# Kernel optimization log

Hardware: AMD Instinct MI355X
Metric: run time of the kernel (lower is better)

The kernel has to match this reference:

```python
import jax, jax.numpy as jnp
import numpy as np

N_NODES = 100000
N_EDGES = 1600000
D_IN = 128
D_HID = 128
N_LAYERS = 3


def setup_inputs() -> dict:
    key = jax.random.key(0)
    k1, k2, k3, k4 = jax.random.split(key, 4)
    x = jax.random.normal(k1, (N_NODES, D_IN), dtype=jnp.float32)
    edge_index = jax.random.randint(k2, (2, N_EDGES), 0, N_NODES, dtype=jnp.int64)
    # Glorot-ish scale for stability across 3 layers
    Ws = jax.random.normal(k3, (N_LAYERS, D_IN, D_HID), dtype=jnp.float32) * (1.0 / np.sqrt(D_IN))
    bs = jax.random.normal(k4, (N_LAYERS, D_HID), dtype=jnp.float32) * 0.01
    return {"x": x, "edge_index": edge_index, "Ws": Ws, "bs": bs}


def _gcn_conv(x, row, col, deg_inv_sqrt, W, b, n_nodes):
    # Linear transform first (PyG GCNConv), then gather-normalize-scatter.
    h = x @ W                                        # [N, D]
    norm = deg_inv_sqrt[row] * deg_inv_sqrt[col]     # [E+N] (self-loops included)
    msg = h[row] * norm[:, None]                     # gather + scale, [E+N, D]
    out = jax.ops.segment_sum(msg, col, num_segments=n_nodes)  # scatter-add
    return out + b


def reference(x, edge_index, Ws, bs):
    n = x.shape[0]
    # add self-loops once (same for every layer)
    loop = jnp.arange(n, dtype=edge_index.dtype)
    row = jnp.concatenate([edge_index[0], loop])
    col = jnp.concatenate([edge_index[1], loop])
    # symmetric normalization: deg over target nodes (incl. self-loops)
    deg = jax.ops.segment_sum(jnp.ones_like(col, dtype=x.dtype), col, num_segments=n)
    deg_inv_sqrt = jnp.where(deg > 0, jax.lax.rsqrt(jnp.maximum(deg, 1.0)), 0.0)
    h = x
    for i in range(Ws.shape[0]):
        h = jax.nn.relu(_gcn_conv(h, row, col, deg_inv_sqrt, Ws[i], bs[i], n))
    return h
```

## Files before the change

### kernel.cpp

```cpp
#include <hip/hip_runtime.h>
#include <hip/hip_bf16.h>

#define NN 100000
#define NROWS 100032
#define NE 1600000
#define DD 128
#define NBUK 196
#define F1_BLOCKS 256
#define F3_BLOCKS 256

typedef unsigned short ushort_t;
typedef unsigned int uint_t;
typedef unsigned long long uint64_t_;
typedef __attribute__((ext_vector_type(8))) short bf16x8;
typedef __attribute__((ext_vector_type(4))) float f32x4;

__device__ __forceinline__ ushort_t bf16rne(float f) {
    uint_t u = __float_as_uint(f);
    u += 0x7FFF + ((u >> 16) & 1);
    return (ushort_t)(u >> 16);
}
__device__ __forceinline__ float bfLo(uint_t u) { return __uint_as_float(u << 16); }
__device__ __forceinline__ float bfHi(uint_t u) { return __uint_as_float(u & 0xFFFF0000u); }


__global__ __launch_bounds__(256) void f1_bucket_count(const int* __restrict__ col,
                                                       int* __restrict__ bukCount) {
    __shared__ int hist[NBUK];
    for (int t = threadIdx.x; t < NBUK; t += 256) hist[t] = 0;
    __syncthreads();
    const int epb = (NE + F1_BLOCKS - 1) / F1_BLOCKS;
    const int e0 = blockIdx.x * epb;
    const int e1 = min(e0 + epb, NE);
    for (int e = e0 + threadIdx.x; e < e1; e += 256)
        atomicAdd(&hist[col[e] >> 9], 1);
    __syncthreads();
    for (int t = threadIdx.x; t < NBUK; t += 256)
        if (hist[t]) atomicAdd(&bukCount[t], hist[t]);
}

__global__ void f2_bucket_scan(const int* __restrict__ bukCount,
                               int* __restrict__ bukBase,
                               int* __restrict__ bukCursor,
                               int* __restrict__ offsets) {
    __shared__ int s[256];
    const int t = threadIdx.x;
    int v = (t < NBUK) ? bukCount[t] : 0;
    s[t] = v;
    __syncthreads();
    for (int off = 1; off < 256; off <<= 1) {
        int tmp = (t >= off) ? s[t - off] : 0;
        __syncthreads();
        s[t] += tmp;
        __syncthreads();
    }
    int excl = s[t] - v;
    if (t < NBUK) { bukBase[t] = excl; bukCursor[t] = excl; }
    if (t == 255) { bukBase[NBUK] = s[255]; offsets[NN] = s[255]; }
}

__global__ __launch_bounds__(256) void f3_scatter(const int* __restrict__ row,
                                                  const int* __restrict__ col,
                                                  int* __restrict__ bukCursor,
                                                  int* __restrict__ ebuf) {
    __shared__ int hist[4][NBUK];
    __shared__ int base[4][NBUK];
    const int t = threadIdx.x;
    const int w = t >> 6;
    const int lane = t & 63;
    for (int i = t; i < 4 * NBUK; i += 256) (&hist[0][0])[i] = 0;
    __syncthreads();
    const int epb = (NE + F3_BLOCKS - 1) / F3_BLOCKS;
    const int e0 = blockIdx.x * epb;
    const int e1 = min(e0 + epb, NE);
    const int wepb = (e1 - e0 + 3) >> 2;
    const int we0 = e0 + w * wepb;
    const int we1 = min(we0 + wepb, e1);
    for (int e = we0 + lane; e < we1; e += 64)
        atomicAdd(&hist[w][col[e] >> 9], 1);
    __syncthreads();
    if (t < NBUK) {
        int h0 = hist[0][t], h1 = hist[1][t], h2 = hist[2][t], h3 = hist[3][t];
        int tot = h0 + h1 + h2 + h3;
        int g = tot ? atomicAdd(&bukCursor[t], tot) : 0;
        base[0][t] = g; base[1][t] = g + h0;
        base[2][t] = g + h0 + h1; base[3][t] = g + h0 + h1 + h2;
        hist[0][t] = 0; hist[1][t] = 0; hist[2][t] = 0; hist[3][t] = 0;
    }
    __syncthreads();
    for (int e = we0 + lane; e < we1; e += 64) {
        int c = col[e];
        int b = c >> 9;
        int r = atomicAdd(&hist[w][b], 1);
        ebuf[base[w][b] + r] = (row[e] << 9) | (c & 511);
    }
}

__global__ __launch_bounds__(256) void f4_finalize(const int* __restrict__ ebuf,
                                                   const int* __restrict__ bukBase,
                                                   int* __restrict__ offsets,
                                                   float* __restrict__ dis,
                                                   int* __restrict__ csr_src) {
    __shared__ int cnt[512];
    __shared__ int cur[512];
    __shared__ int s[256];
    const int t = threadIdx.x;
    const int colBase = blockIdx.x << 9;
    const int ncols = min(512, NN - colBase);
    cnt[t] = 0; cnt[t + 256] = 0;
    __syncthreads();
    const int eb0 = bukBase[blockIdx.x];
    const int eb1 = bukBase[blockIdx.x + 1];
    for (int e = eb0 + t; e < eb1; e += 256)
        atomicAdd(&cnt[ebuf[e] & 511], 1);
    __syncthreads();
    const int c0 = cnt[2 * t], c1 = cnt[2 * t + 1];
    const int psum = c0 + c1;
    s[t] = psum;
    __syncthreads();
    for (int off = 1; off < 256; off <<= 1) {
        int tmp = (t >= off) ? s[t - off] : 0;
        __syncthreads();
        s[t] += tmp;
        __syncthreads();
    }
    const int exclPair = s[t] - psum;
    const int g0 = eb0 + exclPair;
    const int g1 = g0 + c0;
    cur[2 * t] = g0; cur[2 * t + 1] = g1;
    if (2 * t < ncols)     { offsets[colBase + 2 * t]     = g0; dis[colBase + 2 * t]     = rsqrtf((float)(c0 + 1)); }
    if (2 * t + 1 < ncols) { offsets[colBase + 2 * t + 1] = g1; dis[colBase + 2 * t + 1] = rsqrtf((float)(c1 + 1)); }
    __syncthreads();
    for (int e = eb0 + t; e < eb1; e += 256) {
        int pc = ebuf[e];
        int p = atomicAdd(&cur[pc & 511], 1);
        csr_src[p] = pc >> 9;
    }
}


__global__ __launch_bounds__(256) void wt_kernel(const float* __restrict__ Ws,
                                                 ushort_t* __restrict__ wT) {
    int idx = blockIdx.x * 256 + threadIdx.x;
    if (idx >= 3 * 128 * 16) return;
    int l = idx >> 11;
    int r = idx & 2047;
    int c = r >> 4;
    int kc = r & 15;
    const float* w = Ws + l * 16384;
    ushort_t tmp[8];
#pragma unroll
    for (int e = 0; e < 8; ++e)
        tmp[e] = bf16rne(w[(kc * 8 + e) * 128 + c]);
    *(uint4*)&wT[(size_t)l * 16384 + c * 128 + kc * 8] = *(uint4*)tmp;
}


template<bool XF32>
__global__ __launch_bounds__(256) void gemm_mfma(const void* __restrict__ Xv,
                                                 const ushort_t* __restrict__ wT,
                                                 const float* __restrict__ dis,
                                                 ushort_t* __restrict__ Y) {
    __shared__ short smem[128 * 136];
    {
        const uint4* src = (const uint4*)wT;
        int t = threadIdx.x;
#pragma unroll
        for (int i = 0; i < 8; ++i) {
            int idx = i * 256 + t;
            int rowc = idx >> 4;
            int kc = idx & 15;
            uint4 v = src[idx];
            *(uint4*)&smem[rowc * 136 + kc * 8] = v;
        }
    }
    __syncthreads();

    const int wave = threadIdx.x >> 6;
    const int lane = threadIdx.x & 63;
    const int m = lane & 15;
    const int kg = lane >> 4;
    const int r0 = blockIdx.x * 64 + wave * 16;
    const int rowA = min(r0 + m, NN - 1);

    f32x4 acc[8];
#pragma unroll
    for (int ct = 0; ct < 8; ++ct) acc[ct] = (f32x4){0.f, 0.f, 0.f, 0.f};

#pragma unroll
    for (int ks = 0; ks < 4; ++ks) {
        bf16x8 af;
        if (XF32) {
            const float* xp = (const float*)Xv + (size_t)rowA * DD + ks * 32 + kg * 8;
            float4 f0 = *(const float4*)xp;
            float4 f1 = *(const float4*)(xp + 4);
            af[0] = (short)bf16rne(f0.x); af[1] = (short)bf16rne(f0.y);
            af[2] = (short)bf16rne(f0.z); af[3] = (short)bf16rne(f0.w);
            af[4] = (short)bf16rne(f1.x); af[5] = (short)bf16rne(f1.y);
            af[6] = (short)bf16rne(f1.z); af[7] = (short)bf16rne(f1.w);
        } else {
            const ushort_t* xp = (const ushort_t*)Xv + (size_t)rowA * DD + ks * 32 + kg * 8;
            af = *(const bf16x8*)xp;
        }
#pragma unroll
        for (int ct = 0; ct < 8; ++ct) {
            bf16x8 bf = *(const bf16x8*)&smem[(ct * 16 + m) * 136 + ks * 32 + kg * 8];
            acc[ct] = __builtin_amdgcn_mfma_f32_16x16x32_bf16(af, bf, acc[ct], 0, 0, 0);
        }
    }

    __syncthreads();

    ushort_t* sl = (ushort_t*)smem;
    const int rbase = r0 + kg * 4;
    float dv[4];
#pragma unroll
    for (int rg = 0; rg < 4; ++rg) dv[rg] = dis[min(rbase + rg, NN - 1)];
#pragma unroll
    for (int ct = 0; ct < 8; ++ct) {
#pragma unroll
        for (int rg = 0; rg < 4; ++rg)
            sl[(wave * 16 + kg * 4 + rg) * 132 + ct * 16 + m] = bf16rne(acc[ct][rg] * dv[rg]);
    }

    const int i = threadIdx.x >> 2;
    const int q = threadIdx.x & 3;
    const int grow = blockIdx.x * 64 + i;
    const bool ok = grow < NN;
    const ushort_t* rb = sl + i * 132;
    uint64_t_* lp2 = (uint64_t_*)Y;
#pragma unroll
    for (int s = 0; s < 8; ++s) {
        const uint_t* p = (const uint_t*)(rb + s * 16 + q * 4);
        uint64_t_ d = (uint64_t_)p[0] | ((uint64_t_)p[1] << 32);
        uint64_t_ z = ok ? d : 0ull;
        __builtin_nontemporal_store(z, &lp2[((size_t)s * NROWS + grow) * 4 + q]);
    }
}


template<bool F32OUT>
__global__ __launch_bounds__(256) void agg_kernel(const uint_t* __restrict__ lin_planes,
                                                  const int* __restrict__ offsets,
                                                  const int* __restrict__ csr_src,
                                                  const float* __restrict__ dis,
                                                  const float* __restrict__ bias,
                                                  void* __restrict__ outv) {
    const int bid  = blockIdx.x;
    const int s    = bid & 7;
    const int gblk = bid >> 3;
    const int w    = threadIdx.x >> 6;
    const int lane = threadIdx.x & 63;
    const int g    = lane >> 3;
    const int u    = lane & 7;
    const int v    = gblk * 32 + w * 8 + g;

    const int start = offsets[v];
    const int deg   = offsets[v + 1] - start;

    const uint_t* plane = lin_planes + (size_t)s * (NROWS * 8);

    int iv[4];
    {
        const int* cp = csr_src + start + u;
        int i0 = cp[0];
        int i1 = cp[8];
        int i2 = cp[16];
        int i3 = cp[24];
        iv[0] = (u      < deg) ? i0 : NN;
        iv[1] = (u +  8 < deg) ? i1 : NN;
        iv[2] = (u + 16 < deg) ? i2 : NN;
        iv[3] = (u + 24 < deg) ? i3 : NN;
    }

    int wmax = deg;
    wmax = max(wmax, __shfl_xor(wmax, 8));
    wmax = max(wmax, __shfl_xor(wmax, 16));
    wmax = max(wmax, __shfl_xor(wmax, 32));

    float accx = 0.f, accy = 0.f;
    const int gbase = lane & 56;
#pragma unroll
    for (int b = 0; b < 4; ++b) {
        if (b * 8 < wmax) {
#pragma unroll
            for (int jj = 0; jj < 8; ++jj) {
                int src = __shfl(iv[b], gbase + jj);
                uint_t a = plane[((uint_t)src << 3) + u];
                accx += bfLo(a); accy += bfHi(a);
            }
        }
    }
    {
        uint_t a = plane[((uint_t)v << 3) + u];
        accx += bfLo(a); accy += bfHi(a);
    }
    if (deg > 32) {
        for (int e = start + 32; e < start + deg; ++e) {
            int src = csr_src[e];
            uint_t a = plane[((uint_t)src << 3) + u];
            accx += bfLo(a); accy += bfHi(a);
        }
    }

    const float dv = dis[v];
    const float2 b2 = ((const float2*)bias)[s * 8 + u];
    float rx = fmaxf(fmaf(dv, accx, b2.x), 0.f);
    float ry = fmaxf(fmaf(dv, accy, b2.y), 0.f);
    const size_t oidx = (size_t)v * 64 + s * 8 + u;
    if (F32OUT) {
        float2 o = make_float2(rx, ry);
        __builtin_nontemporal_store(*(const uint64_t_*)&o, (uint64_t_*)((float2*)outv + oidx));
    } else {
        uint_t pk = (uint_t)bf16rne(rx) | ((uint_t)bf16rne(ry) << 16);
        __builtin_nontemporal_store(pk, (uint_t*)outv + oidx);
    }
}


extern "C" void kernel_launch(void* const* d_in, const int* in_sizes, int n_in,
                              void* d_out, int out_size, void* d_ws, size_t ws_size,
                              hipStream_t stream) {
    const float* x   = (const float*)d_in[0];
    const int*   ei  = (const int*)d_in[1];
    const float* Ws  = (const float*)d_in[2];
    const float* bs  = (const float*)d_in[3];

    const int* row = ei;
    const int* col = ei + NE;

    char* ws = (char*)d_ws;
    ushort_t* lin    = (ushort_t*)(ws + 0);
    int*   ebuf      = (int*)  (ws + 0);
    ushort_t* hb     = (ushort_t*)(ws + 25608192);
    float* dis       = (float*)(ws + 51208192);
    int*   offsets   = (int*)  (ws + 51608192);
    int*   csr_src   = (int*)  (ws + 52008208);
    int*   bukCount  = (int*)  (ws + 58408208);
    int*   bukBase   = (int*)  (ws + 58409008);
    int*   bukCursor = (int*)  (ws + 58409808);
    ushort_t* wT     = (ushort_t*)(ws + 58410608);

    (void)hipMemsetAsync(bukCount, 0, NBUK * sizeof(int), stream);
    f1_bucket_count<<<F1_BLOCKS, 256, 0, stream>>>(col, bukCount);
    f2_bucket_scan<<<1, 256, 0, stream>>>(bukCount, bukBase, bukCursor, offsets);
    f3_scatter<<<F3_BLOCKS, 256, 0, stream>>>(row, col, bukCursor, ebuf);
    f4_finalize<<<NBUK, 256, 0, stream>>>(ebuf, bukBase, offsets, dis, csr_src);
    wt_kernel<<<24, 256, 0, stream>>>(Ws, wT);

    const int gemmGrid = NROWS / 64;
    const int aggGrid = (NN / 32) * 8;
    gemm_mfma<true><<<gemmGrid, 256, 0, stream>>>(x, wT, dis, lin);
    agg_kernel<false><<<aggGrid, 256, 0, stream>>>((const uint_t*)lin, offsets, csr_src, dis, bs, hb);
    gemm_mfma<false><<<gemmGrid, 256, 0, stream>>>(hb, wT + 16384, dis, lin);
    agg_kernel<false><<<aggGrid, 256, 0, stream>>>((const uint_t*)lin, offsets, csr_src, dis, bs + DD, hb);
    gemm_mfma<false><<<gemmGrid, 256, 0, stream>>>(hb, wT + 32768, dis, lin);
    agg_kernel<true><<<aggGrid, 256, 0, stream>>>((const uint_t*)lin, offsets, csr_src, dis, bs + 2 * DD, d_out);
}
```

Measured before the change: 324.5 us.

## Widen feature slices to 32 columns and pair XCDs per slice in aggregation

The intermediate linear output is re-laid out from 8 planes of 16 bf16 columns into 4 planes of 32 columns, so each gathered neighbor row fragment becomes 64 bytes and each lane loads 8 bytes instead of 4. The aggregation grid is remapped so two XCDs share each slice plane, which keeps per-XCD L2 locality while halving the number of gather passes over the edge list. It trades a larger per-XCD working set (each plane is twice as big) for fewer index reads and wider, more efficient gather transactions.

```diff
diff --git a/kernel.cpp b/kernel.cpp
--- a/kernel.cpp
+++ b/kernel.cpp
@@ -8,6 +8,7 @@
 #define NBUK 196
 #define F1_BLOCKS 256
 #define F3_BLOCKS 256
+#define NGBLK 3125
 
 typedef unsigned short ushort_t;
 typedef unsigned int uint_t;
@@ -228,27 +229,31 @@
     const int grow = blockIdx.x * 64 + i;
     const bool ok = grow < NN;
     const ushort_t* rb = sl + i * 132;
-    uint64_t_* lp2 = (uint64_t_*)Y;
-#pragma unroll
-    for (int s = 0; s < 8; ++s) {
-        const uint_t* p = (const uint_t*)(rb + s * 16 + q * 4);
-        uint64_t_ d = (uint64_t_)p[0] | ((uint64_t_)p[1] << 32);
-        uint64_t_ z = ok ? d : 0ull;
-        __builtin_nontemporal_store(z, &lp2[((size_t)s * NROWS + grow) * 4 + q]);
+#pragma unroll
+    for (int s = 0; s < 4; ++s) {
+        const uint_t* p = (const uint_t*)(rb + s * 32 + q * 8);
+        uint64_t_ d0 = (uint64_t_)p[0] | ((uint64_t_)p[1] << 32);
+        uint64_t_ d1 = (uint64_t_)p[2] | ((uint64_t_)p[3] << 32);
+        if (!ok) { d0 = 0ull; d1 = 0ull; }
+        uint64_t_* dst = (uint64_t_*)((char*)Y + ((size_t)s * NROWS + grow) * 64 + q * 16);
+        __builtin_nontemporal_store(d0, dst);
+        __builtin_nontemporal_store(d1, dst + 1);
     }
 }
 
 
 template<bool F32OUT>
-__global__ __launch_bounds__(256) void agg_kernel(const uint_t* __restrict__ lin_planes,
+__global__ __launch_bounds__(256) void agg_kernel(const uint_t* __restrict__ lin_sl,
                                                   const int* __restrict__ offsets,
                                                   const int* __restrict__ csr_src,
                                                   const float* __restrict__ dis,
                                                   const float* __restrict__ bias,
                                                   void* __restrict__ outv) {
     const int bid  = blockIdx.x;
-    const int s    = bid & 7;
-    const int gblk = bid >> 3;
+    const int xcd  = bid & 7;
+    const int sli  = xcd >> 1;
+    const int gblk = (bid >> 3) * 2 + (xcd & 1);
+    if (gblk >= NGBLK) return;
     const int w    = threadIdx.x >> 6;
     const int lane = threadIdx.x & 63;
     const int g    = lane >> 3;
@@ -258,7 +263,7 @@
     const int start = offsets[v];
     const int deg   = offsets[v + 1] - start;
 
-    const uint_t* plane = lin_planes + (size_t)s * (NROWS * 8);
+    const uint_t* plane = lin_sl + (size_t)sli * (NROWS * 16);
 
     int iv[4];
     {
@@ -278,7 +283,7 @@
     wmax = max(wmax, __shfl_xor(wmax, 16));
     wmax = max(wmax, __shfl_xor(wmax, 32));
 
-    float accx = 0.f, accy = 0.f;
+    float a0 = 0.f, a1 = 0.f, a2 = 0.f, a3 = 0.f;
     const int gbase = lane & 56;
 #pragma unroll
     for (int b = 0; b < 4; ++b) {
@@ -286,34 +291,43 @@
 #pragma unroll
             for (int jj = 0; jj < 8; ++jj) {
                 int src = __shfl(iv[b], gbase + jj);
-                uint_t a = plane[((uint_t)src << 3) + u];
-                accx += bfLo(a); accy += bfHi(a);
+                uint2 a = *(const uint2*)(plane + ((size_t)src << 4) + u * 2);
+                a0 += bfLo(a.x); a1 += bfHi(a.x);
+                a2 += bfLo(a.y); a3 += bfHi(a.y);
             }
         }
     }
     {
-        uint_t a = plane[((uint_t)v << 3) + u];
-        accx += bfLo(a); accy += bfHi(a);
+        uint2 a = *(const uint2*)(plane + ((size_t)v << 4) + u * 2);
+        a0 += bfLo(a.x); a1 += bfHi(a.x);
+        a2 += bfLo(a.y); a3 += bfHi(a.y);
     }
     if (deg > 32) {
         for (int e = start + 32; e < start + deg; ++e) {
             int src = csr_src[e];
-            uint_t a = plane[((uint_t)src << 3) + u];
-            accx += bfLo(a); accy += bfHi(a);
+            uint2 a = *(const uint2*)(plane + ((size_t)src << 4) + u * 2);
+            a0 += bfLo(a.x); a1 += bfHi(a.x);
+            a2 += bfLo(a.y); a3 += bfHi(a.y);
         }
     }
 
     const float dv = dis[v];
-    const float2 b2 = ((const float2*)bias)[s * 8 + u];
-    float rx = fmaxf(fmaf(dv, accx, b2.x), 0.f);
-    float ry = fmaxf(fmaf(dv, accy, b2.y), 0.f);
-    const size_t oidx = (size_t)v * 64 + s * 8 + u;
+    const float4 b4 = ((const float4*)bias)[sli * 8 + u];
+    float r0 = fmaxf(fmaf(dv, a0, b4.x), 0.f);
+    float r1 = fmaxf(fmaf(dv, a1, b4.y), 0.f);
+    float r2 = fmaxf(fmaf(dv, a2, b4.z), 0.f);
+    float r3 = fmaxf(fmaf(dv, a3, b4.w), 0.f);
     if (F32OUT) {
-        float2 o = make_float2(rx, ry);
-        __builtin_nontemporal_store(*(const uint64_t_*)&o, (uint64_t_*)((float2*)outv + oidx));
+        float* op = (float*)outv + (size_t)v * DD + sli * 32 + u * 4;
+        float2 lo = make_float2(r0, r1);
+        float2 hi = make_float2(r2, r3);
+        __builtin_nontemporal_store(*(const uint64_t_*)&lo, (uint64_t_*)op);
+        __builtin_nontemporal_store(*(const uint64_t_*)&hi, (uint64_t_*)op + 1);
     } else {
-        uint_t pk = (uint_t)bf16rne(rx) | ((uint_t)bf16rne(ry) << 16);
-        __builtin_nontemporal_store(pk, (uint_t*)outv + oidx);
+        uint_t p0 = (uint_t)bf16rne(r0) | ((uint_t)bf16rne(r1) << 16);
+        uint_t p1 = (uint_t)bf16rne(r2) | ((uint_t)bf16rne(r3) << 16);
+        uint64_t_ pk = (uint64_t_)p0 | ((uint64_t_)p1 << 32);
+        __builtin_nontemporal_store(pk, (uint64_t_*)((uint_t*)outv + (size_t)v * 64 + sli * 16 + u * 2));
     }
 }
 
@@ -349,7 +363,7 @@
     wt_kernel<<<24, 256, 0, stream>>>(Ws, wT);
 
     const int gemmGrid = NROWS / 64;
-    const int aggGrid = (NN / 32) * 8;
+    const int aggGrid = ((NGBLK + 1) / 2) * 8;
     gemm_mfma<true><<<gemmGrid, 256, 0, stream>>>(x, wT, dis, lin);
     agg_kernel<false><<<aggGrid, 256, 0, stream>>>((const uint_t*)lin, offsets, csr_src, dis, bs, hb);
     gemm_mfma<false><<<gemmGrid, 256, 0, stream>>>(hb, wT + 16384, dis, lin);
```

Result: faster. 300.8 us (-7.3%).
